# Kernel optimization log

Hardware: AMD Instinct MI355X
Metric: run time of the kernel (lower is better)

The kernel has to match this reference:

```python
import jax, jax.numpy as jnp
import numpy as np

B, N_SITES, N_BONDS = 16, 2048, 65536
SITE_LEN, BOND_LEN, STATE_LEN = 64, 64, 64
H1, H2 = 256, 256


def setup_inputs() -> dict:
    key = jax.random.key(0)
    ks = jax.random.split(key, 10)
    d_in = SITE_LEN + BOND_LEN + STATE_LEN
    s = lambda fan_in: 1.0 / np.sqrt(fan_in)
    return {
        "sites": jax.random.normal(ks[0], (B, N_SITES, SITE_LEN), jnp.float32),
        "bonds": jax.random.normal(ks[1], (B, N_BONDS, BOND_LEN), jnp.float32),
        "states": jax.random.normal(ks[2], (B, STATE_LEN), jnp.float32),
        "indices1": jax.random.randint(ks[3], (N_BONDS,), 0, N_SITES),
        "W1": jax.random.uniform(ks[4], (d_in, H1), jnp.float32, -s(d_in), s(d_in)),
        "b1": jnp.zeros((H1,), jnp.float32),
        "W2": jax.random.uniform(ks[5], (H1, H2), jnp.float32, -s(H1), s(H1)),
        "b2": jnp.zeros((H2,), jnp.float32),
        "W3": jax.random.uniform(ks[6], (H2, SITE_LEN), jnp.float32, -s(H2), s(H2)),
        "b3": jnp.zeros((SITE_LEN,), jnp.float32),
    }


def reference(sites, bonds, states, indices1, W1, b1, W2, b2, W3, b3):
    n_sites = sites.shape[1]
    # scatter_mean over the bond axis (dim=1). indices shared across batch, so
    # put bonds axis leading and use a single segment_sum: [n_bonds, B, bond_len]
    seg_sum = jax.ops.segment_sum(jnp.swapaxes(bonds, 0, 1), indices1,
                                  num_segments=n_sites)          # [n_sites, B, bond_len]
    counts = jax.ops.segment_sum(jnp.ones((bonds.shape[1],), bonds.dtype),
                                 indices1, num_segments=n_sites)  # [n_sites]
    denom = jnp.maximum(counts, 1.0)[:, None, None]
    bonds_pool = jnp.swapaxes(seg_sum / denom, 0, 1)              # [B, n_sites, bond_len]
    states1 = jnp.broadcast_to(states[:, None, :],
                               (sites.shape[0], n_sites, states.shape[-1]))
    v = jnp.concatenate([bonds_pool, sites, states1], axis=2)
    h = jax.nn.relu(v @ W1 + b1)
    h = jax.nn.relu(h @ W2 + b2)
    return jax.nn.relu(h @ W3 + b3)
```

## Files before the change

### kernel.cpp

```cpp
#include <hip/hip_runtime.h>
#include <cstdint>
#include <cstddef>

typedef _Float16 f16;
typedef f16 f16x8 __attribute__((ext_vector_type(8)));
typedef f16 f16x4 __attribute__((ext_vector_type(4)));
typedef float f32x4 __attribute__((ext_vector_type(4)));

constexpr int NS = 2048;
constexpr int NB = 65536;

__global__ void count_kernel(const int* __restrict__ idx, int* __restrict__ counts) {
    int i = blockIdx.x * 256 + threadIdx.x;
    atomicAdd(&counts[idx[i]], 1);
}

__global__ void scan_kernel(const int* __restrict__ counts, int* __restrict__ offsets) {
    int l = threadIdx.x;
    int c[32]; int run = 0;
    #pragma unroll
    for (int i = 0; i < 32; ++i) { c[i] = run; run += counts[l * 32 + i]; }
    int incl = run;
    #pragma unroll
    for (int d = 1; d < 64; d <<= 1) { int v = __shfl_up(incl, d); if (l >= d) incl += v; }
    int excl = incl - run;
    #pragma unroll
    for (int i = 0; i < 32; ++i) offsets[l * 32 + i] = excl + c[i];
}

__global__ void fill_kernel(const int* __restrict__ idx, const int* __restrict__ offsets,
                            int* __restrict__ cursor, int* __restrict__ bucket) {
    int i = blockIdx.x * 256 + threadIdx.x;
    int s = idx[i];
    int pos = atomicAdd(&cursor[s], 1);
    bucket[offsets[s] + pos] = i;
}

__global__ __launch_bounds__(256) void pool_kernel(const float* __restrict__ bonds,
                                                   const int* __restrict__ counts,
                                                   const int* __restrict__ offsets,
                                                   const int* __restrict__ bucket,
                                                   float* __restrict__ pool) {
    int s = blockIdx.x;
    int t = threadIdx.x;
    int b = t >> 4, f4 = t & 15;
    int cnt = counts[s], start = offsets[s];
    f32x4 acc = {0.f, 0.f, 0.f, 0.f};
    const f32x4* base = reinterpret_cast<const f32x4*>(bonds) + (size_t)b * NB * 16;
    int i = 0;
    for (; i + 4 <= cnt; i += 4) {
        int id0 = bucket[start + i + 0];
        int id1 = bucket[start + i + 1];
        int id2 = bucket[start + i + 2];
        int id3 = bucket[start + i + 3];
        f32x4 v0 = base[(size_t)id0 * 16 + f4];
        f32x4 v1 = base[(size_t)id1 * 16 + f4];
        f32x4 v2 = base[(size_t)id2 * 16 + f4];
        f32x4 v3 = base[(size_t)id3 * 16 + f4];
        acc += v0; acc += v1; acc += v2; acc += v3;
    }
    for (; i < cnt; ++i) {
        int id = bucket[start + i];
        acc += base[(size_t)id * 16 + f4];
    }
    float inv = 1.0f / (float)(cnt > 1 ? cnt : 1);
    acc *= inv;
    reinterpret_cast<f32x4*>(pool)[((size_t)b * NS + s) * 16 + f4] = acc;
}

__global__ void pack_kernel(const float* __restrict__ W1, const float* __restrict__ W2,
                            const float* __restrict__ W3, f16* __restrict__ pw1,
                            f16* __restrict__ pw2, f16* __restrict__ pw3) {
    int t = blockIdx.x * 256 + threadIdx.x;
    int tt = t >> 6, l = t & 63;
    const float* W; f16* dst; int N, tloc, kt, nt;
    if (tt < 96)       { W = W1; dst = pw1; N = 256; tloc = tt;       kt = tloc >> 4; nt = tloc & 15; }
    else if (tt < 224) { W = W2; dst = pw2; N = 256; tloc = tt - 96;  kt = tloc >> 4; nt = tloc & 15; }
    else               { W = W3; dst = pw3; N = 64;  tloc = tt - 224; kt = tloc >> 2; nt = tloc & 3;  }
    int kbase = kt * 32 + (l >> 4) * 8;
    int n = nt * 16 + (l & 15);
    f16x8 o;
    #pragma unroll
    for (int j = 0; j < 8; ++j) o[j] = (f16)W[(size_t)(kbase + j) * N + n];
    *reinterpret_cast<f16x8*>(&dst[(size_t)(tloc * 64 + l) * 8]) = o;
}

__global__ __launch_bounds__(256, 4) void mlp_kernel(
    const float* __restrict__ pool, const float* __restrict__ sites, const float* __restrict__ states,
    const float* __restrict__ b1, const float* __restrict__ b2, const float* __restrict__ b3,
    const f16x8* __restrict__ pw1, const f16x8* __restrict__ pw2, const f16x8* __restrict__ pw3,
    float* __restrict__ out) {
    constexpr int STR = 280;
    __shared__ f16 bufA[32 * STR];
    __shared__ f16 bufB[32 * STR];
    int t = threadIdx.x;
    int w = t >> 6, lane = t & 63;
    int arow = lane & 15, ag = lane >> 4;
    int m0 = blockIdx.x * 32;
    int b = m0 >> 11;

    {
        const float* srcs[3] = { pool + (size_t)m0 * 64,
                                 sites + (size_t)m0 * 64,
                                 states + (size_t)b * 64 };
        #pragma unroll
        for (int seg = 0; seg < 3; ++seg) {
            #pragma unroll
            for (int p = 0; p < 2; ++p) {
                int i = p * 256 + t;
                int row = i >> 4, c4 = i & 15;
                const float* sp = srcs[seg] + (seg == 2 ? (size_t)0 : (size_t)row * 64) + c4 * 4;
                f32x4 v = *reinterpret_cast<const f32x4*>(sp);
                f16x4 h = { (f16)v[0], (f16)v[1], (f16)v[2], (f16)v[3] };
                *reinterpret_cast<f16x4*>(&bufA[row * STR + seg * 64 + c4 * 4]) = h;
            }
        }
    }
    __syncthreads();

    {
        f32x4 acc[2][4];
        #pragma unroll
        for (int ni = 0; ni < 4; ++ni) {
            float bv = b1[w * 64 + ni * 16 + arow];
            acc[0][ni] = f32x4{bv, bv, bv, bv};
            acc[1][ni] = f32x4{bv, bv, bv, bv};
        }
        #pragma unroll
        for (int kt = 0; kt < 6; ++kt) {
            f16x8 af[2], bfr[4];
            #pragma unroll
            for (int mi = 0; mi < 2; ++mi)
                af[mi] = *reinterpret_cast<const f16x8*>(&bufA[(mi * 16 + arow) * STR + kt * 32 + ag * 8]);
            #pragma unroll
            for (int ni = 0; ni < 4; ++ni) bfr[ni] = pw1[(kt * 16 + w * 4 + ni) * 64 + lane];
            #pragma unroll
            for (int mi = 0; mi < 2; ++mi)
                #pragma unroll
                for (int ni = 0; ni < 4; ++ni)
                    acc[mi][ni] = __builtin_amdgcn_mfma_f32_16x16x32_f16(af[mi], bfr[ni], acc[mi][ni], 0, 0, 0);
        }
        #pragma unroll
        for (int mi = 0; mi < 2; ++mi)
            #pragma unroll
            for (int ni = 0; ni < 4; ++ni)
                #pragma unroll
                for (int j = 0; j < 4; ++j) {
                    float x = acc[mi][ni][j]; x = x > 0.f ? x : 0.f;
                    bufB[(mi * 16 + ag * 4 + j) * STR + w * 64 + ni * 16 + arow] = (f16)x;
                }
    }
    __syncthreads();

    {
        f32x4 acc[2][4];
        #pragma unroll
        for (int ni = 0; ni < 4; ++ni) {
            float bv = b2[w * 64 + ni * 16 + arow];
            acc[0][ni] = f32x4{bv, bv, bv, bv};
            acc[1][ni] = f32x4{bv, bv, bv, bv};
        }
        #pragma unroll
        for (int kt = 0; kt < 8; ++kt) {
            f16x8 af[2], bfr[4];
            #pragma unroll
            for (int mi = 0; mi < 2; ++mi)
                af[mi] = *reinterpret_cast<const f16x8*>(&bufB[(mi * 16 + arow) * STR + kt * 32 + ag * 8]);
            #pragma unroll
            for (int ni = 0; ni < 4; ++ni) bfr[ni] = pw2[(kt * 16 + w * 4 + ni) * 64 + lane];
            #pragma unroll
            for (int mi = 0; mi < 2; ++mi)
                #pragma unroll
                for (int ni = 0; ni < 4; ++ni)
                    acc[mi][ni] = __builtin_amdgcn_mfma_f32_16x16x32_f16(af[mi], bfr[ni], acc[mi][ni], 0, 0, 0);
        }
        #pragma unroll
        for (int mi = 0; mi < 2; ++mi)
            #pragma unroll
            for (int ni = 0; ni < 4; ++ni)
                #pragma unroll
                for (int j = 0; j < 4; ++j) {
                    float x = acc[mi][ni][j]; x = x > 0.f ? x : 0.f;
                    bufA[(mi * 16 + ag * 4 + j) * STR + w * 64 + ni * 16 + arow] = (f16)x;
                }
    }
    __syncthreads();

    {
        f32x4 acc[2];
        float bv = b3[w * 16 + arow];
        acc[0] = f32x4{bv, bv, bv, bv};
        acc[1] = f32x4{bv, bv, bv, bv};
        #pragma unroll
        for (int kt = 0; kt < 8; ++kt) {
            f16x8 bfr = pw3[(kt * 4 + w) * 64 + lane];
            #pragma unroll
            for (int mi = 0; mi < 2; ++mi) {
                f16x8 af = *reinterpret_cast<const f16x8*>(&bufA[(mi * 16 + arow) * STR + kt * 32 + ag * 8]);
                acc[mi] = __builtin_amdgcn_mfma_f32_16x16x32_f16(af, bfr, acc[mi], 0, 0, 0);
            }
        }
        #pragma unroll
        for (int mi = 0; mi < 2; ++mi)
            #pragma unroll
            for (int j = 0; j < 4; ++j) {
                float x = acc[mi][j]; x = x > 0.f ? x : 0.f;
                out[(size_t)(m0 + mi * 16 + ag * 4 + j) * 64 + w * 16 + arow] = x;
            }
    }
}

extern "C" void kernel_launch(void* const* d_in, const int* in_sizes, int n_in,
                              void* d_out, int out_size, void* d_ws, size_t ws_size,
                              hipStream_t stream) {
    (void)in_sizes; (void)n_in; (void)out_size; (void)ws_size;
    const float* sites  = (const float*)d_in[0];
    const float* bonds  = (const float*)d_in[1];
    const float* states = (const float*)d_in[2];
    const int*   idx    = (const int*)d_in[3];
    const float* W1 = (const float*)d_in[4];
    const float* b1 = (const float*)d_in[5];
    const float* W2 = (const float*)d_in[6];
    const float* b2 = (const float*)d_in[7];
    const float* W3 = (const float*)d_in[8];
    const float* b3 = (const float*)d_in[9];
    float* out = (float*)d_out;

    char* ws = (char*)d_ws;
    int* counts  = (int*)(ws + 0);
    int* cursor  = (int*)(ws + 8192);
    int* offsets = (int*)(ws + 16384);
    int* bucket  = (int*)(ws + 24576);
    float* pool  = (float*)(ws + 24576 + 262144);
    f16* pw1     = (f16*)(ws + 24576 + 262144 + 8388608);
    f16* pw2     = pw1 + 96 * 512;
    f16* pw3     = pw2 + 128 * 512;

    hipMemsetAsync(counts, 0, 16384, stream);
    pack_kernel<<<64, 256, 0, stream>>>(W1, W2, W3, pw1, pw2, pw3);
    count_kernel<<<256, 256, 0, stream>>>(idx, counts);
    scan_kernel<<<1, 64, 0, stream>>>(counts, offsets);
    fill_kernel<<<256, 256, 0, stream>>>(idx, offsets, cursor, bucket);
    pool_kernel<<<2048, 256, 0, stream>>>(bonds, counts, offsets, bucket, pool);
    mlp_kernel<<<1024, 256, 0, stream>>>(pool, sites, states, b1, b2, b3,
                                         (const f16x8*)pw1, (const f16x8*)pw2, (const f16x8*)pw3, out);
}
```

Measured before the change: 92.43 us.

## Fuse scatter-mean pooling into MLP kernel and merge pack with count

The gather-and-average pooling over bonds now runs inside the MLP kernel, writing the averaged rows directly into shared memory as fp16. This drops the 8 MB intermediate pool buffer and its write and read back, and removes one launch. Weight packing and bond counting are also merged into a single launch. In exchange, the pooling work is spread over only 1024 blocks that also hold MLP resources (launch bounds 4 per CU), instead of 2048 dedicated blocks, and the irregular per-site counts may stall the MLP warps.

```diff
diff --git a/kernel.cpp b/kernel.cpp
--- a/kernel.cpp
+++ b/kernel.cpp
@@ -10,9 +10,27 @@
 constexpr int NS = 2048;
 constexpr int NB = 65536;
 
-__global__ void count_kernel(const int* __restrict__ idx, int* __restrict__ counts) {
-    int i = blockIdx.x * 256 + threadIdx.x;
-    atomicAdd(&counts[idx[i]], 1);
+__global__ void pack_count_kernel(const float* __restrict__ W1, const float* __restrict__ W2,
+                                  const float* __restrict__ W3, f16* __restrict__ pw1,
+                                  f16* __restrict__ pw2, f16* __restrict__ pw3,
+                                  const int* __restrict__ idx, int* __restrict__ counts) {
+    if (blockIdx.x < 64) {
+        int t = blockIdx.x * 256 + threadIdx.x;
+        int tt = t >> 6, l = t & 63;
+        const float* W; f16* dst; int N, tloc, kt, nt;
+        if (tt < 96)       { W = W1; dst = pw1; N = 256; tloc = tt;       kt = tloc >> 4; nt = tloc & 15; }
+        else if (tt < 224) { W = W2; dst = pw2; N = 256; tloc = tt - 96;  kt = tloc >> 4; nt = tloc & 15; }
+        else               { W = W3; dst = pw3; N = 64;  tloc = tt - 224; kt = tloc >> 2; nt = tloc & 3;  }
+        int kbase = kt * 32 + (l >> 4) * 8;
+        int n = nt * 16 + (l & 15);
+        f16x8 o;
+        #pragma unroll
+        for (int j = 0; j < 8; ++j) o[j] = (f16)W[(size_t)(kbase + j) * N + n];
+        *reinterpret_cast<f16x8*>(&dst[(size_t)(tloc * 64 + l) * 8]) = o;
+    } else {
+        int i = (blockIdx.x - 64) * 256 + threadIdx.x;
+        atomicAdd(&counts[idx[i]], 1);
+    }
 }
 
 __global__ void scan_kernel(const int* __restrict__ counts, int* __restrict__ offsets) {
@@ -36,57 +54,9 @@
     bucket[offsets[s] + pos] = i;
 }
 
-__global__ __launch_bounds__(256) void pool_kernel(const float* __restrict__ bonds,
-                                                   const int* __restrict__ counts,
-                                                   const int* __restrict__ offsets,
-                                                   const int* __restrict__ bucket,
-                                                   float* __restrict__ pool) {
-    int s = blockIdx.x;
-    int t = threadIdx.x;
-    int b = t >> 4, f4 = t & 15;
-    int cnt = counts[s], start = offsets[s];
-    f32x4 acc = {0.f, 0.f, 0.f, 0.f};
-    const f32x4* base = reinterpret_cast<const f32x4*>(bonds) + (size_t)b * NB * 16;
-    int i = 0;
-    for (; i + 4 <= cnt; i += 4) {
-        int id0 = bucket[start + i + 0];
-        int id1 = bucket[start + i + 1];
-        int id2 = bucket[start + i + 2];
-        int id3 = bucket[start + i + 3];
-        f32x4 v0 = base[(size_t)id0 * 16 + f4];
-        f32x4 v1 = base[(size_t)id1 * 16 + f4];
-        f32x4 v2 = base[(size_t)id2 * 16 + f4];
-        f32x4 v3 = base[(size_t)id3 * 16 + f4];
-        acc += v0; acc += v1; acc += v2; acc += v3;
-    }
-    for (; i < cnt; ++i) {
-        int id = bucket[start + i];
-        acc += base[(size_t)id * 16 + f4];
-    }
-    float inv = 1.0f / (float)(cnt > 1 ? cnt : 1);
-    acc *= inv;
-    reinterpret_cast<f32x4*>(pool)[((size_t)b * NS + s) * 16 + f4] = acc;
-}
-
-__global__ void pack_kernel(const float* __restrict__ W1, const float* __restrict__ W2,
-                            const float* __restrict__ W3, f16* __restrict__ pw1,
-                            f16* __restrict__ pw2, f16* __restrict__ pw3) {
-    int t = blockIdx.x * 256 + threadIdx.x;
-    int tt = t >> 6, l = t & 63;
-    const float* W; f16* dst; int N, tloc, kt, nt;
-    if (tt < 96)       { W = W1; dst = pw1; N = 256; tloc = tt;       kt = tloc >> 4; nt = tloc & 15; }
-    else if (tt < 224) { W = W2; dst = pw2; N = 256; tloc = tt - 96;  kt = tloc >> 4; nt = tloc & 15; }
-    else               { W = W3; dst = pw3; N = 64;  tloc = tt - 224; kt = tloc >> 2; nt = tloc & 3;  }
-    int kbase = kt * 32 + (l >> 4) * 8;
-    int n = nt * 16 + (l & 15);
-    f16x8 o;
-    #pragma unroll
-    for (int j = 0; j < 8; ++j) o[j] = (f16)W[(size_t)(kbase + j) * N + n];
-    *reinterpret_cast<f16x8*>(&dst[(size_t)(tloc * 64 + l) * 8]) = o;
-}
-
-__global__ __launch_bounds__(256, 4) void mlp_kernel(
-    const float* __restrict__ pool, const float* __restrict__ sites, const float* __restrict__ states,
+__global__ __launch_bounds__(256, 4) void fused_kernel(
+    const float* __restrict__ bonds, const float* __restrict__ sites, const float* __restrict__ states,
+    const int* __restrict__ counts, const int* __restrict__ offsets, const int* __restrict__ bucket,
     const float* __restrict__ b1, const float* __restrict__ b2, const float* __restrict__ b3,
     const f16x8* __restrict__ pw1, const f16x8* __restrict__ pw2, const f16x8* __restrict__ pw3,
     float* __restrict__ out) {
@@ -96,24 +66,57 @@
     int t = threadIdx.x;
     int w = t >> 6, lane = t & 63;
     int arow = lane & 15, ag = lane >> 4;
-    int m0 = blockIdx.x * 32;
-    int b = m0 >> 11;
-
-    {
-        const float* srcs[3] = { pool + (size_t)m0 * 64,
-                                 sites + (size_t)m0 * 64,
-                                 states + (size_t)b * 64 };
-        #pragma unroll
-        for (int seg = 0; seg < 3; ++seg) {
-            #pragma unroll
-            for (int p = 0; p < 2; ++p) {
-                int i = p * 256 + t;
-                int row = i >> 4, c4 = i & 15;
-                const float* sp = srcs[seg] + (seg == 2 ? (size_t)0 : (size_t)row * 64) + c4 * 4;
-                f32x4 v = *reinterpret_cast<const f32x4*>(sp);
-                f16x4 h = { (f16)v[0], (f16)v[1], (f16)v[2], (f16)v[3] };
-                *reinterpret_cast<f16x4*>(&bufA[row * STR + seg * 64 + c4 * 4]) = h;
-            }
+    int blk = blockIdx.x;
+    int b = blk >> 6;
+    int s0 = (blk & 63) * 32;
+    int m0 = b * NS + s0;
+
+    {
+        int slot = t >> 4, f4 = t & 15;
+        const f32x4* base = reinterpret_cast<const f32x4*>(bonds) + (size_t)b * NB * 16;
+        #pragma unroll
+        for (int sg = 0; sg < 2; ++sg) {
+            int srow = sg * 16 + slot;
+            int s = s0 + srow;
+            int cnt = counts[s], start = offsets[s];
+            f32x4 acc = {0.f, 0.f, 0.f, 0.f};
+            int i = 0;
+            for (; i + 4 <= cnt; i += 4) {
+                int id0 = bucket[start + i + 0];
+                int id1 = bucket[start + i + 1];
+                int id2 = bucket[start + i + 2];
+                int id3 = bucket[start + i + 3];
+                f32x4 v0 = base[(size_t)id0 * 16 + f4];
+                f32x4 v1 = base[(size_t)id1 * 16 + f4];
+                f32x4 v2 = base[(size_t)id2 * 16 + f4];
+                f32x4 v3 = base[(size_t)id3 * 16 + f4];
+                acc += v0; acc += v1; acc += v2; acc += v3;
+            }
+            for (; i < cnt; ++i) {
+                int id = bucket[start + i];
+                acc += base[(size_t)id * 16 + f4];
+            }
+            float inv = 1.0f / (float)(cnt > 1 ? cnt : 1);
+            acc *= inv;
+            f16x4 h = { (f16)acc[0], (f16)acc[1], (f16)acc[2], (f16)acc[3] };
+            *reinterpret_cast<f16x4*>(&bufA[srow * STR + f4 * 4]) = h;
+        }
+    }
+    {
+        #pragma unroll
+        for (int p = 0; p < 2; ++p) {
+            int i = p * 256 + t;
+            int row = i >> 4, c4 = i & 15;
+            f32x4 v = *reinterpret_cast<const f32x4*>(sites + (size_t)(m0 + row) * 64 + c4 * 4);
+            f16x4 h = { (f16)v[0], (f16)v[1], (f16)v[2], (f16)v[3] };
+            *reinterpret_cast<f16x4*>(&bufA[row * STR + 64 + c4 * 4]) = h;
+        }
+        f32x4 v = *reinterpret_cast<const f32x4*>(states + (size_t)b * 64 + (t & 15) * 4);
+        f16x4 h = { (f16)v[0], (f16)v[1], (f16)v[2], (f16)v[3] };
+        #pragma unroll
+        for (int p = 0; p < 2; ++p) {
+            int row = p * 16 + (t >> 4), c4 = t & 15;
+            *reinterpret_cast<f16x4*>(&bufA[row * STR + 128 + c4 * 4]) = h;
         }
     }
     __syncthreads();
@@ -231,17 +234,15 @@
     int* cursor  = (int*)(ws + 8192);
     int* offsets = (int*)(ws + 16384);
     int* bucket  = (int*)(ws + 24576);
-    float* pool  = (float*)(ws + 24576 + 262144);
-    f16* pw1     = (f16*)(ws + 24576 + 262144 + 8388608);
+    f16* pw1     = (f16*)(ws + 24576 + 262144);
     f16* pw2     = pw1 + 96 * 512;
     f16* pw3     = pw2 + 128 * 512;
 
     hipMemsetAsync(counts, 0, 16384, stream);
-    pack_kernel<<<64, 256, 0, stream>>>(W1, W2, W3, pw1, pw2, pw3);
-    count_kernel<<<256, 256, 0, stream>>>(idx, counts);
+    pack_count_kernel<<<320, 256, 0, stream>>>(W1, W2, W3, pw1, pw2, pw3, idx, counts);
     scan_kernel<<<1, 64, 0, stream>>>(counts, offsets);
     fill_kernel<<<256, 256, 0, stream>>>(idx, offsets, cursor, bucket);
-    pool_kernel<<<2048, 256, 0, stream>>>(bonds, counts, offsets, bucket, pool);
-    mlp_kernel<<<1024, 256, 0, stream>>>(pool, sites, states, b1, b2, b3,
-                                         (const f16x8*)pw1, (const f16x8*)pw2, (const f16x8*)pw3, out);
-}
+    fused_kernel<<<1024, 256, 0, stream>>>(bonds, sites, states, counts, offsets, bucket,
+                                           b1, b2, b3,
+                                           (const f16x8*)pw1, (const f16x8*)pw2, (const f16x8*)pw3, out);
+}
```

Result: faster. 86.78 us (-6.1%).
